# Optimization experiments

Hardware: AMD Instinct MI355X
Metric: run time of the kernel (lower is better)

The kernel has to match this reference:

```python
import jax, jax.numpy as jnp
import numpy as np

EPS = 1e-5
N_POINTS = 262144
K_VOL = 27
N_PAIRS = 65536
C_IN = 64
C_OUT = 64


def setup_inputs() -> dict:
    key = jax.random.key(0)
    k1, k2, k3, k4 = jax.random.split(key, 4)
    std = 1.0 / np.sqrt(C_IN * K_VOL)  # matches reset_parameters uniform(-std, std)
    input_feat = jax.random.normal(k1, (N_POINTS, C_IN), dtype=jnp.float32)
    input_coord = jax.random.randint(k2, (N_POINTS, 4), 0, 1024, dtype=jnp.int32)
    input_cmap = jnp.arange(N_POINTS, dtype=jnp.int32)
    input_kmap = jax.random.randint(k3, (K_VOL, N_PAIRS, 2), 0, N_POINTS, dtype=jnp.int32)
    weight = jax.random.uniform(k4, (K_VOL, C_IN, C_OUT), dtype=jnp.float32,
                                minval=-std, maxval=std)
    bn_weight = jnp.ones((C_OUT,), dtype=jnp.float32)
    bn_bias = jnp.zeros((C_OUT,), dtype=jnp.float32)
    return {
        "input_feat": input_feat,
        "input_coord": input_coord,
        "input_cmap": input_cmap,
        "input_kmap": input_kmap,
        "weight": weight,
        "bn_weight": bn_weight,
        "bn_bias": bn_bias,
    }


def reference(input_feat, input_coord, input_cmap, input_kmap, weight, bn_weight, bn_bias):
    # Sparse 3D conv (stride=1 -> output coords == input coords) via
    # gather -> per-offset GEMM -> scatter-add, then training-mode BN + ReLU.
    n_out = input_feat.shape[0]
    in_idx = input_kmap[..., 0]   # [K, P]
    out_idx = input_kmap[..., 1]  # [K, P]
    gathered = input_feat[in_idx]                         # [K, P, Cin]
    partial = jnp.einsum('kpc,kcd->kpd', gathered, weight)  # [K, P, Cout]
    out = jax.ops.segment_sum(partial.reshape(-1, partial.shape[-1]),
                              out_idx.reshape(-1), num_segments=n_out)  # [N, Cout]
    # BatchNorm1d, training mode (batch statistics, biased variance)
    mean = jnp.mean(out, axis=0)
    var = jnp.var(out, axis=0)
    y = (out - mean) * jax.lax.rsqrt(var + EPS) * bn_weight + bn_bias
    return jax.nn.relu(y)
```

## Files before the change

kernel.cpp:

```cpp
#include <hip/hip_runtime.h>

#define NPTS 262144
#define KVOL 27
#define NPAIRS 65536
#define TP (KVOL*NPAIRS)
#define CH 64
#define NT32 (NPTS/32)
#define NSEG (NT32*32)
#define NBLK2 2048
#define MAXR 12

typedef __attribute__((ext_vector_type(8))) short bf16x8;
typedef __attribute__((ext_vector_type(4))) float f32x4;

__device__ inline unsigned short f2bf(float x){
  unsigned int u = __float_as_uint(x);
  u += 0x7FFFu + ((u >> 16) & 1u);
  return (unsigned short)(u >> 16);
}

__device__ inline bf16x8 pack8(float4 a, float4 b){
  bf16x8 r;
  r[0]=(short)f2bf(a.x); r[1]=(short)f2bf(a.y); r[2]=(short)f2bf(a.z); r[3]=(short)f2bf(a.w);
  r[4]=(short)f2bf(b.x); r[5]=(short)f2bf(b.y); r[6]=(short)f2bf(b.z); r[7]=(short)f2bf(b.w);
  return r;
}

template<bool BF16G>
__global__ void k_pre(const float* __restrict__ feat, const float* __restrict__ w,
                      const int2* __restrict__ km, unsigned short* __restrict__ featb,
                      unsigned short* __restrict__ wpack, int* __restrict__ cnt,
                      unsigned short* __restrict__ rankb){
  int i = blockIdx.x*256 + threadIdx.x;
  if (BF16G){
    float4 v = ((const float4*)feat)[i];
    ushort4 r;
    r.x = f2bf(v.x); r.y = f2bf(v.y); r.z = f2bf(v.z); r.w = f2bf(v.w);
    ((ushort4*)featb)[i] = r;
  }
  if (i < TP){
    int2 io = km[i];
    int k = i >> 16;
    int seg = ((io.y >> 5) << 5) | k;
    int rank = atomicAdd(&cnt[seg], 1);
    rankb[i] = (unsigned short)rank;
  }
  if (i < KVOL*CH*CH){
    int j = i & 7, col = (i >> 3) & 63, kb = (i >> 9) & 7, k = i >> 12;
    wpack[i] = f2bf(w[(k*CH + kb*8 + j)*CH + col]);
  }
}

__global__ void k_assign(const int* __restrict__ cnt, int* __restrict__ gtot,
                         int2* __restrict__ segd){
  int i = blockIdx.x*256 + threadIdx.x;
  int l = threadIdx.x & 63;
  int c = cnt[i];
  int v = c;
  #pragma unroll
  for (int d = 1; d < 64; d <<= 1){ int u = __shfl_up(v, d, 64); if (l >= d) v += u; }
  int wtot = __shfl(v, 63, 64);
  int base = 0;
  if (l == 63) base = atomicAdd(gtot, wtot);
  base = __shfl(base, 63, 64);
  segd[i] = make_int2(base + v - c, c);
}

__global__ void k_scatter(const int2* __restrict__ km, const unsigned short* __restrict__ rankb,
                          const int2* __restrict__ segd, int* __restrict__ records){
  int i = blockIdx.x*256 + threadIdx.x;
  int2 io = km[i];
  int k = i >> 16;
  int seg = ((io.y >> 5) << 5) | k;
  int pos = segd[seg].x + rankb[i];
  records[pos] = io.x | ((io.y & 31) << 18);
}

template<bool BF16G>
__global__ __launch_bounds__(256, 4) void k_conv8(
    const unsigned short* __restrict__ featb, const float* __restrict__ featf,
    const unsigned short* __restrict__ wpack, const int* __restrict__ records,
    const int2* __restrict__ segd, float* __restrict__ out, float* __restrict__ partials)
{
  __shared__ int lcnt[4][32];
  __shared__ int lslot[4][MAXR*32];
  __shared__ float sred[4][2][64];

  int tid = threadIdx.x;
  int wv = tid>>6, l = tid&63, lg = l>>4, li = l&15;
  int t32 = blockIdx.x*4 + wv;
  int segbase = t32 << 5;

  const bf16x8* fb = (const bf16x8*)featb;
  const float4* ff = (const float4*)featf;
  const bf16x8* wbase = ((const bf16x8*)wpack) + lg*64 + li;

  f32x4 acc[2][4];
  #pragma unroll
  for (int rt = 0; rt < 2; rt++)
    #pragma unroll
    for (int ct = 0; ct < 4; ct++) acc[rt][ct] = (f32x4)(0.0f);

  int2 sd  = segd[segbase];
  int2 sd1 = segd[segbase + 1];
  int rec_pf = 0;
  if (l < sd.y) rec_pf = records[sd.x + l];

  for (int k = 0; k < KVOL; k++){
    int2 sd2 = segd[segbase + min(k + 2, 31)];
    int rec_nx = 0;
    if (l < sd1.y) rec_nx = records[sd1.x + l];

    int beg = sd.x, tot = sd.y;
    if (tot > 0){
      bf16x8 B[4][2];
      #pragma unroll
      for (int ct = 0; ct < 4; ct++)
        #pragma unroll
        for (int h = 0; h < 2; h++)
          B[ct][h] = wbase[k*512 + h*256 + ct*16];

      int rec = rec_pf;
      for (int c0 = 0; c0 < tot; c0 += 64){
        int cc = min(64, tot - c0);
        if (c0 > 0 && l < cc) rec = records[beg + c0 + l];
        if (l < 32) lcnt[wv][l] = 0;
        if (l < cc){
          int slot = (rec >> 18) & 31;
          int rank = atomicAdd(&lcnt[wv][slot], 1);
          if (rank < MAXR) lslot[wv][rank*32 + slot] = rec;
        }
        int cnt0 = min(lcnt[wv][li], MAXR);
        int cnt1 = min(lcnt[wv][16 + li], MAXR);
        int nr = max(cnt0, cnt1);
        #pragma unroll
        for (int d = 1; d < 16; d <<= 1) nr = max(nr, __shfl_xor(nr, d, 64));

        for (int rb = 0; rb < nr; rb += 2){
          int recA0 = lslot[wv][rb*32 + li];
          int recA1 = lslot[wv][rb*32 + 16 + li];
          int recB0 = lslot[wv][min(rb+1, MAXR-1)*32 + li];
          int recB1 = lslot[wv][min(rb+1, MAXR-1)*32 + 16 + li];
          bool vA0 = (rb < cnt0), vA1 = (rb < cnt1);
          bool vB0 = (rb+1 < cnt0), vB1 = (rb+1 < cnt1);
          bf16x8 a00 = (bf16x8)(short)0, a01 = (bf16x8)(short)0;
          bf16x8 a10 = (bf16x8)(short)0, a11 = (bf16x8)(short)0;
          bf16x8 b00 = (bf16x8)(short)0, b01 = (bf16x8)(short)0;
          bf16x8 b10 = (bf16x8)(short)0, b11 = (bf16x8)(short)0;
          if (vA0){
            int in = recA0 & 0x3FFFF;
            if (BF16G){ a00 = fb[in*8 + lg]; a01 = fb[in*8 + 4 + lg]; }
            else {
              float4 u0 = ff[in*16 + lg*2],     u1 = ff[in*16 + lg*2 + 1];
              float4 u2 = ff[in*16 + 8 + lg*2], u3 = ff[in*16 + 8 + lg*2 + 1];
              a00 = pack8(u0, u1); a01 = pack8(u2, u3);
            }
          }
          if (vA1){
            int in = recA1 & 0x3FFFF;
            if (BF16G){ a10 = fb[in*8 + lg]; a11 = fb[in*8 + 4 + lg]; }
            else {
              float4 u0 = ff[in*16 + lg*2],     u1 = ff[in*16 + lg*2 + 1];
              float4 u2 = ff[in*16 + 8 + lg*2], u3 = ff[in*16 + 8 + lg*2 + 1];
              a10 = pack8(u0, u1); a11 = pack8(u2, u3);
            }
          }
          if (vB0){
            int in = recB0 & 0x3FFFF;
            if (BF16G){ b00 = fb[in*8 + lg]; b01 = fb[in*8 + 4 + lg]; }
            else {
              float4 u0 = ff[in*16 + lg*2],     u1 = ff[in*16 + lg*2 + 1];
              float4 u2 = ff[in*16 + 8 + lg*2], u3 = ff[in*16 + 8 + lg*2 + 1];
              b00 = pack8(u0, u1); b01 = pack8(u2, u3);
            }
          }
          if (vB1){
            int in = recB1 & 0x3FFFF;
            if (BF16G){ b10 = fb[in*8 + lg]; b11 = fb[in*8 + 4 + lg]; }
            else {
              float4 u0 = ff[in*16 + lg*2],     u1 = ff[in*16 + lg*2 + 1];
              float4 u2 = ff[in*16 + 8 + lg*2], u3 = ff[in*16 + 8 + lg*2 + 1];
              b10 = pack8(u0, u1); b11 = pack8(u2, u3);
            }
          }
          if (__ballot(vA0)){
            #pragma unroll
            for (int ct = 0; ct < 4; ct++){
              acc[0][ct] = __builtin_amdgcn_mfma_f32_16x16x32_bf16(a00, B[ct][0], acc[0][ct], 0, 0, 0);
              acc[0][ct] = __builtin_amdgcn_mfma_f32_16x16x32_bf16(a01, B[ct][1], acc[0][ct], 0, 0, 0);
            }
          }
          if (__ballot(vA1)){
            #pragma unroll
            for (int ct = 0; ct < 4; ct++){
              acc[1][ct] = __builtin_amdgcn_mfma_f32_16x16x32_bf16(a10, B[ct][0], acc[1][ct], 0, 0, 0);
              acc[1][ct] = __builtin_amdgcn_mfma_f32_16x16x32_bf16(a11, B[ct][1], acc[1][ct], 0, 0, 0);
            }
          }
          if (rb + 1 < nr){
            if (__ballot(vB0)){
              #pragma unroll
              for (int ct = 0; ct < 4; ct++){
                acc[0][ct] = __builtin_amdgcn_mfma_f32_16x16x32_bf16(b00, B[ct][0], acc[0][ct], 0, 0, 0);
                acc[0][ct] = __builtin_amdgcn_mfma_f32_16x16x32_bf16(b01, B[ct][1], acc[0][ct], 0, 0, 0);
              }
            }
            if (__ballot(vB1)){
              #pragma unroll
              for (int ct = 0; ct < 4; ct++){
                acc[1][ct] = __builtin_amdgcn_mfma_f32_16x16x32_bf16(b10, B[ct][0], acc[1][ct], 0, 0, 0);
                acc[1][ct] = __builtin_amdgcn_mfma_f32_16x16x32_bf16(b11, B[ct][1], acc[1][ct], 0, 0, 0);
              }
            }
          }
        }
      }
    }
    rec_pf = rec_nx; sd = sd1; sd1 = sd2;
  }

  #pragma unroll
  for (int rt = 0; rt < 2; rt++)
    #pragma unroll
    for (int r = 0; r < 4; r++){
      int row = t32*32 + rt*16 + lg*4 + r;
      #pragma unroll
      for (int ct = 0; ct < 4; ct++)
        out[row*CH + ct*16 + li] = acc[rt][ct][r];
    }

  float s1[4], s2[4];
  #pragma unroll
  for (int ct = 0; ct < 4; ct++){
    float a1 = 0.f, a2 = 0.f;
    #pragma unroll
    for (int rt = 0; rt < 2; rt++)
      #pragma unroll
      for (int r = 0; r < 4; r++){
        float v = acc[rt][ct][r];
        a1 += v; a2 += v*v;
      }
    a1 += __shfl_xor(a1, 16, 64); a1 += __shfl_xor(a1, 32, 64);
    a2 += __shfl_xor(a2, 16, 64); a2 += __shfl_xor(a2, 32, 64);
    s1[ct] = a1; s2[ct] = a2;
  }
  __syncthreads();
  if (l < 16){
    #pragma unroll
    for (int ct = 0; ct < 4; ct++){
      sred[wv][0][ct*16 + li] = s1[ct];
      sred[wv][1][ct*16 + li] = s2[ct];
    }
  }
  __syncthreads();
  if (tid < 128){
    int h = tid >> 6, c = tid & 63;
    float p = sred[0][h][c] + sred[1][h][c] + sred[2][h][c] + sred[3][h][c];
    partials[blockIdx.x*128 + tid] = p;
  }
}

__global__ void k_statred(const float* __restrict__ partials, float* __restrict__ stats){
  __shared__ float sm_[256];
  int c = blockIdx.x;
  int t = threadIdx.x;
  float s = 0.f;
  for (int b = t; b < NBLK2; b += 256) s += partials[b*128 + c];
  sm_[t] = s;
  __syncthreads();
  for (int d = 128; d > 0; d >>= 1){
    if (t < d) sm_[t] += sm_[t+d];
    __syncthreads();
  }
  if (t == 0) stats[c] = sm_[0];
}

__global__ void k_bn(float* __restrict__ out, const float* __restrict__ stats,
                     const float* __restrict__ g, const float* __restrict__ b){
  int i = blockIdx.x * blockDim.x + threadIdx.x;
  float4 v = ((const float4*)out)[i];
  int c0 = (i * 4) & 63;
  float vals[4] = {v.x, v.y, v.z, v.w};
  float res[4];
  #pragma unroll
  for (int q = 0; q < 4; q++){
    int c = c0 + q;
    float mean = stats[c] * (1.0f/NPTS);
    float var  = stats[64+c] * (1.0f/NPTS) - mean*mean;
    float inv  = rsqrtf(var + 1e-5f);
    float y = (vals[q] - mean) * inv * g[c] + b[c];
    res[q] = fmaxf(y, 0.0f);
  }
  float4 r; r.x=res[0]; r.y=res[1]; r.z=res[2]; r.w=res[3];
  ((float4*)out)[i] = r;
}

extern "C" void kernel_launch(void* const* d_in, const int* in_sizes, int n_in,
                              void* d_out, int out_size, void* d_ws, size_t ws_size,
                              hipStream_t stream) {
  const float* feat   = (const float*)d_in[0];
  const int*   kmap   = (const int*)d_in[3];
  const float* weight = (const float*)d_in[4];
  const float* bnw    = (const float*)d_in[5];
  const float* bnb    = (const float*)d_in[6];
  float* out = (float*)d_out;

  char* ws = (char*)d_ws;
  size_t cur = 0;
  auto take = [&](size_t bytes){
    cur = (cur + 255) & ~(size_t)255;
    size_t p = cur; cur += bytes; return p;
  };
  float* stats          = (float*)(ws + take(2*CH*sizeof(float)));
  float* partials       = (float*)(ws + take((size_t)NBLK2*128*sizeof(float)));
  int* cnt              = (int*)(ws + take((size_t)(NSEG+64)*4));
  int2* segd            = (int2*)(ws + take((size_t)NSEG*8));
  unsigned short* wpack = (unsigned short*)(ws + take((size_t)KVOL*CH*CH*2));
  unsigned short* rankb = (unsigned short*)(ws + take((size_t)TP*2));
  int* records          = (int*)(ws + take((size_t)TP*4));
  size_t featb_off      = take((size_t)NPTS*CH*2);
  bool useBf16 = (ws_size >= cur);
  unsigned short* featb = (unsigned short*)(ws + featb_off);
  int* gtot = cnt + NSEG;

  hipMemsetAsync(cnt, 0, (size_t)(NSEG+64)*4, stream);

  const int2* km = (const int2*)kmap;
  if (useBf16)
    k_pre<true><<<NPTS*CH/4/256, 256, 0, stream>>>(feat, weight, km, featb, wpack, cnt, rankb);
  else
    k_pre<false><<<TP/256, 256, 0, stream>>>(feat, weight, km, featb, wpack, cnt, rankb);

  k_assign<<<NSEG/256, 256, 0, stream>>>(cnt, gtot, segd);
  k_scatter<<<TP/256, 256, 0, stream>>>(km, rankb, segd, records);

  if (useBf16)
    k_conv8<true><<<NBLK2, 256, 0, stream>>>(featb, feat, wpack, records, segd, out, partials);
  else
    k_conv8<false><<<NBLK2, 256, 0, stream>>>(featb, feat, wpack, records, segd, out, partials);

  k_statred<<<128, 256, 0, stream>>>(partials, stats);
  k_bn<<<NPTS*CH/4/256, 256, 0, stream>>>(out, stats, bnw, bnb);
}
```

Baseline: 315.1 us.

## Switch conv tile MFMA from 16x16x32 to 32x32x16 over full 32-row tile

```diff
diff --git a/kernel.cpp b/kernel.cpp
--- a/kernel.cpp
+++ b/kernel.cpp
@@ -11,7 +11,7 @@
 #define MAXR 12
 
 typedef __attribute__((ext_vector_type(8))) short bf16x8;
-typedef __attribute__((ext_vector_type(4))) float f32x4;
+typedef __attribute__((ext_vector_type(16))) float f32x16;
 
 __device__ inline unsigned short f2bf(float x){
   unsigned int u = __float_as_uint(x);
@@ -46,8 +46,9 @@
     rankb[i] = (unsigned short)rank;
   }
   if (i < KVOL*CH*CH){
-    int j = i & 7, col = (i >> 3) & 63, kb = (i >> 9) & 7, k = i >> 12;
-    wpack[i] = f2bf(w[(k*CH + kb*8 + j)*CH + col]);
+    int j = i & 7, col = (i >> 3) & 63, kh = (i >> 9) & 1, ks = (i >> 10) & 3, k = i >> 12;
+    int cin = ks*16 + kh*8 + j;
+    wpack[i] = f2bf(w[(k*CH + cin)*CH + col]);
   }
 }
 
@@ -77,7 +78,7 @@
 }
 
 template<bool BF16G>
-__global__ __launch_bounds__(256, 4) void k_conv8(
+__global__ __launch_bounds__(256, 4) void k_conv9(
     const unsigned short* __restrict__ featb, const float* __restrict__ featf,
     const unsigned short* __restrict__ wpack, const int* __restrict__ records,
     const int2* __restrict__ segd, float* __restrict__ out, float* __restrict__ partials)
@@ -87,19 +88,15 @@
   __shared__ float sred[4][2][64];
 
   int tid = threadIdx.x;
-  int wv = tid>>6, l = tid&63, lg = l>>4, li = l&15;
+  int wv = tid>>6, l = tid&63, ls = l&31, kh = l>>5;
   int t32 = blockIdx.x*4 + wv;
   int segbase = t32 << 5;
 
-  const bf16x8* fb = (const bf16x8*)featb;
+  const bf16x8* fa = ((const bf16x8*)featb) + kh;
   const float4* ff = (const float4*)featf;
-  const bf16x8* wbase = ((const bf16x8*)wpack) + lg*64 + li;
-
-  f32x4 acc[2][4];
-  #pragma unroll
-  for (int rt = 0; rt < 2; rt++)
-    #pragma unroll
-    for (int ct = 0; ct < 4; ct++) acc[rt][ct] = (f32x4)(0.0f);
+  const bf16x8* wb = ((const bf16x8*)wpack) + kh*64 + ls;
+
+  f32x16 acc0 = (f32x16)(0.0f), acc1 = (f32x16)(0.0f);
 
   int2 sd  = segd[segbase];
   int2 sd1 = segd[segbase + 1];
@@ -113,12 +110,12 @@
 
     int beg = sd.x, tot = sd.y;
     if (tot > 0){
-      bf16x8 B[4][2];
+      bf16x8 B[2][4];
       #pragma unroll
-      for (int ct = 0; ct < 4; ct++)
+      for (int ct = 0; ct < 2; ct++)
         #pragma unroll
-        for (int h = 0; h < 2; h++)
-          B[ct][h] = wbase[k*512 + h*256 + ct*16];
+        for (int ks = 0; ks < 4; ks++)
+          B[ct][ks] = wb[(k*4 + ks)*128 + ct*32];
 
       int rec = rec_pf;
       for (int c0 = 0; c0 < tot; c0 += 64){
@@ -130,89 +127,35 @@
           int rank = atomicAdd(&lcnt[wv][slot], 1);
           if (rank < MAXR) lslot[wv][rank*32 + slot] = rec;
         }
-        int cnt0 = min(lcnt[wv][li], MAXR);
-        int cnt1 = min(lcnt[wv][16 + li], MAXR);
-        int nr = max(cnt0, cnt1);
-        #pragma unroll
-        for (int d = 1; d < 16; d <<= 1) nr = max(nr, __shfl_xor(nr, d, 64));
-
-        for (int rb = 0; rb < nr; rb += 2){
-          int recA0 = lslot[wv][rb*32 + li];
-          int recA1 = lslot[wv][rb*32 + 16 + li];
-          int recB0 = lslot[wv][min(rb+1, MAXR-1)*32 + li];
-          int recB1 = lslot[wv][min(rb+1, MAXR-1)*32 + 16 + li];
-          bool vA0 = (rb < cnt0), vA1 = (rb < cnt1);
-          bool vB0 = (rb+1 < cnt0), vB1 = (rb+1 < cnt1);
-          bf16x8 a00 = (bf16x8)(short)0, a01 = (bf16x8)(short)0;
-          bf16x8 a10 = (bf16x8)(short)0, a11 = (bf16x8)(short)0;
-          bf16x8 b00 = (bf16x8)(short)0, b01 = (bf16x8)(short)0;
-          bf16x8 b10 = (bf16x8)(short)0, b11 = (bf16x8)(short)0;
-          if (vA0){
-            int in = recA0 & 0x3FFFF;
-            if (BF16G){ a00 = fb[in*8 + lg]; a01 = fb[in*8 + 4 + lg]; }
-            else {
-              float4 u0 = ff[in*16 + lg*2],     u1 = ff[in*16 + lg*2 + 1];
-              float4 u2 = ff[in*16 + 8 + lg*2], u3 = ff[in*16 + 8 + lg*2 + 1];
-              a00 = pack8(u0, u1); a01 = pack8(u2, u3);
+        int cnt_s = min(lcnt[wv][ls], MAXR);
+        for (int r = 0; r < MAXR; r++){
+          bool valid = (r < cnt_s);
+          if (__ballot(valid) == 0ull) break;
+          int rs = lslot[wv][r*32 + ls];
+          bf16x8 A0 = (bf16x8)(short)0, A1 = (bf16x8)(short)0;
+          bf16x8 A2 = (bf16x8)(short)0, A3 = (bf16x8)(short)0;
+          if (valid){
+            int in = rs & 0x3FFFF;
+            if (BF16G){
+              A0 = fa[in*8];     A1 = fa[in*8 + 2];
+              A2 = fa[in*8 + 4]; A3 = fa[in*8 + 6];
+            } else {
+              float4 u0 = ff[in*16 + kh*2],      u1 = ff[in*16 + kh*2 + 1];
+              float4 u2 = ff[in*16 + 4 + kh*2],  u3 = ff[in*16 + 4 + kh*2 + 1];
+              float4 u4 = ff[in*16 + 8 + kh*2],  u5 = ff[in*16 + 8 + kh*2 + 1];
+              float4 u6 = ff[in*16 + 12 + kh*2], u7 = ff[in*16 + 12 + kh*2 + 1];
+              A0 = pack8(u0, u1); A1 = pack8(u2, u3);
+              A2 = pack8(u4, u5); A3 = pack8(u6, u7);
             }
           }
-          if (vA1){
-            int in = recA1 & 0x3FFFF;
-            if (BF16G){ a10 = fb[in*8 + lg]; a11 = fb[in*8 + 4 + lg]; }
-            else {
-              float4 u0 = ff[in*16 + lg*2],     u1 = ff[in*16 + lg*2 + 1];
-              float4 u2 = ff[in*16 + 8 + lg*2], u3 = ff[in*16 + 8 + lg*2 + 1];
-              a10 = pack8(u0, u1); a11 = pack8(u2, u3);
-            }
-          }
-          if (vB0){
-            int in = recB0 & 0x3FFFF;
-            if (BF16G){ b00 = fb[in*8 + lg]; b01 = fb[in*8 + 4 + lg]; }
-            else {
-              float4 u0 = ff[in*16 + lg*2],     u1 = ff[in*16 + lg*2 + 1];
-              float4 u2 = ff[in*16 + 8 + lg*2], u3 = ff[in*16 + 8 + lg*2 + 1];
-              b00 = pack8(u0, u1); b01 = pack8(u2, u3);
-            }
-          }
-          if (vB1){
-            int in = recB1 & 0x3FFFF;
-            if (BF16G){ b10 = fb[in*8 + lg]; b11 = fb[in*8 + 4 + lg]; }
-            else {
-              float4 u0 = ff[in*16 + lg*2],     u1 = ff[in*16 + lg*2 + 1];
-              float4 u2 = ff[in*16 + 8 + lg*2], u3 = ff[in*16 + 8 + lg*2 + 1];
-              b10 = pack8(u0, u1); b11 = pack8(u2, u3);
-            }
-          }
-          if (__ballot(vA0)){
-            #pragma unroll
-            for (int ct = 0; ct < 4; ct++){
-              acc[0][ct] = __builtin_amdgcn_mfma_f32_16x16x32_bf16(a00, B[ct][0], acc[0][ct], 0, 0, 0);
-              acc[0][ct] = __builtin_amdgcn_mfma_f32_16x16x32_bf16(a01, B[ct][1], acc[0][ct], 0, 0, 0);
-            }
-          }
-          if (__ballot(vA1)){
-            #pragma unroll
-            for (int ct = 0; ct < 4; ct++){
-              acc[1][ct] = __builtin_amdgcn_mfma_f32_16x16x32_bf16(a10, B[ct][0], acc[1][ct], 0, 0, 0);
-              acc[1][ct] = __builtin_amdgcn_mfma_f32_16x16x32_bf16(a11, B[ct][1], acc[1][ct], 0, 0, 0);
-            }
-          }
-          if (rb + 1 < nr){
-            if (__ballot(vB0)){
-              #pragma unroll
-              for (int ct = 0; ct < 4; ct++){
-                acc[0][ct] = __builtin_amdgcn_mfma_f32_16x16x32_bf16(b00, B[ct][0], acc[0][ct], 0, 0, 0);
-                acc[0][ct] = __builtin_amdgcn_mfma_f32_16x16x32_bf16(b01, B[ct][1], acc[0][ct], 0, 0, 0);
-              }
-            }
-            if (__ballot(vB1)){
-              #pragma unroll
-              for (int ct = 0; ct < 4; ct++){
-                acc[1][ct] = __builtin_amdgcn_mfma_f32_16x16x32_bf16(b10, B[ct][0], acc[1][ct], 0, 0, 0);
-                acc[1][ct] = __builtin_amdgcn_mfma_f32_16x16x32_bf16(b11, B[ct][1], acc[1][ct], 0, 0, 0);
-              }
-            }
-          }
+          acc0 = __builtin_amdgcn_mfma_f32_32x32x16_bf16(A0, B[0][0], acc0, 0, 0, 0);
+          acc1 = __builtin_amdgcn_mfma_f32_32x32x16_bf16(A0, B[1][0], acc1, 0, 0, 0);
+          acc0 = __builtin_amdgcn_mfma_f32_32x32x16_bf16(A1, B[0][1], acc0, 0, 0, 0);
+          acc1 = __builtin_amdgcn_mfma_f32_32x32x16_bf16(A1, B[1][1], acc1, 0, 0, 0);
+          acc0 = __builtin_amdgcn_mfma_f32_32x32x16_bf16(A2, B[0][2], acc0, 0, 0, 0);
+          acc1 = __builtin_amdgcn_mfma_f32_32x32x16_bf16(A2, B[1][2], acc1, 0, 0, 0);
+          acc0 = __builtin_amdgcn_mfma_f32_32x32x16_bf16(A3, B[0][3], acc0, 0, 0, 0);
+          acc1 = __builtin_amdgcn_mfma_f32_32x32x16_bf16(A3, B[1][3], acc1, 0, 0, 0);
         }
       }
     }
@@ -220,37 +163,27 @@
   }
 
   #pragma unroll
-  for (int rt = 0; rt < 2; rt++)
-    #pragma unroll
-    for (int r = 0; r < 4; r++){
-      int row = t32*32 + rt*16 + lg*4 + r;
-      #pragma unroll
-      for (int ct = 0; ct < 4; ct++)
-        out[row*CH + ct*16 + li] = acc[rt][ct][r];
-    }
-
-  float s1[4], s2[4];
-  #pragma unroll
-  for (int ct = 0; ct < 4; ct++){
-    float a1 = 0.f, a2 = 0.f;
-    #pragma unroll
-    for (int rt = 0; rt < 2; rt++)
-      #pragma unroll
-      for (int r = 0; r < 4; r++){
-        float v = acc[rt][ct][r];
-        a1 += v; a2 += v*v;
-      }
-    a1 += __shfl_xor(a1, 16, 64); a1 += __shfl_xor(a1, 32, 64);
-    a2 += __shfl_xor(a2, 16, 64); a2 += __shfl_xor(a2, 32, 64);
-    s1[ct] = a1; s2[ct] = a2;
-  }
+  for (int p = 0; p < 16; p++){
+    int row = t32*32 + (p & 3) + 8*(p >> 2) + 4*kh;
+    out[row*CH + ls]      = acc0[p];
+    out[row*CH + 32 + ls] = acc1[p];
+  }
+
+  float s10 = 0.f, s20 = 0.f, s11 = 0.f, s21 = 0.f;
+  #pragma unroll
+  for (int p = 0; p < 16; p++){
+    float v0 = acc0[p], v1 = acc1[p];
+    s10 += v0; s20 += v0*v0;
+    s11 += v1; s21 += v1*v1;
+  }
+  s10 += __shfl_xor(s10, 32, 64); s20 += __shfl_xor(s20, 32, 64);
+  s11 += __shfl_xor(s11, 32, 64); s21 += __shfl_xor(s21, 32, 64);
   __syncthreads();
-  if (l < 16){
-    #pragma unroll
-    for (int ct = 0; ct < 4; ct++){
-      sred[wv][0][ct*16 + li] = s1[ct];
-      sred[wv][1][ct*16 + li] = s2[ct];
-    }
+  if (l < 32){
+    sred[wv][0][ls]      = s10;
+    sred[wv][0][32 + ls] = s11;
+    sred[wv][1][ls]      = s20;
+    sred[wv][1][32 + ls] = s21;
   }
   __syncthreads();
   if (tid < 128){
@@ -335,9 +268,9 @@
   k_scatter<<<TP/256, 256, 0, stream>>>(km, rankb, segd, records);
 
   if (useBf16)
-    k_conv8<true><<<NBLK2, 256, 0, stream>>>(featb, feat, wpack, records, segd, out, partials);
+    k_conv9<true><<<NBLK2, 256, 0, stream>>>(featb, feat, wpack, records, segd, out, partials);
   else
-    k_conv8<false><<<NBLK2, 256, 0, stream>>>(featb, feat, wpack, records, segd, out, partials);
+    k_conv9<false><<<NBLK2, 256, 0, stream>>>(featb, feat, wpack, records, segd, out, partials);
 
   k_statred<<<128, 256, 0, stream>>>(partials, stats);
   k_bn<<<NPTS*CH/4/256, 256, 0, stream>>>(out, stats, bnw, bnb);
```

Result: slower. 346.3 us (+9.9%).

## Double-buffer per-offset slot tables and prefetch next offset's first-rank gathers

Applied to the files above, without the earlier changes.

```diff
diff --git a/kernel.cpp b/kernel.cpp
--- a/kernel.cpp
+++ b/kernel.cpp
@@ -77,13 +77,13 @@
 }
 
 template<bool BF16G>
-__global__ __launch_bounds__(256, 4) void k_conv8(
+__global__ __launch_bounds__(256, 4) void k_conv10(
     const unsigned short* __restrict__ featb, const float* __restrict__ featf,
     const unsigned short* __restrict__ wpack, const int* __restrict__ records,
     const int2* __restrict__ segd, float* __restrict__ out, float* __restrict__ partials)
 {
-  __shared__ int lcnt[4][32];
-  __shared__ int lslot[4][MAXR*32];
+  __shared__ int lcnt[4][2][32];
+  __shared__ int lslot[4][2][MAXR*32];
   __shared__ float sred[4][2][64];
 
   int tid = threadIdx.x;
@@ -101,17 +101,64 @@
     #pragma unroll
     for (int ct = 0; ct < 4; ct++) acc[rt][ct] = (f32x4)(0.0f);
 
-  int2 sd  = segd[segbase];
-  int2 sd1 = segd[segbase + 1];
-  int rec_pf = 0;
-  if (l < sd.y) rec_pf = records[sd.x + l];
+  auto buildTable = [&](int buf, int rec, int cc){
+    if (l < 32) lcnt[wv][buf][l] = 0;
+    if (l < cc){
+      int slot = (rec >> 18) & 31;
+      int rank = atomicAdd(&lcnt[wv][buf][slot], 1);
+      if (rank < MAXR) lslot[wv][buf][rank*32 + slot] = rec;
+    }
+  };
+  auto gatherA = [&](int rec, bool v, bf16x8& X0, bf16x8& X1){
+    X0 = (bf16x8)(short)0; X1 = (bf16x8)(short)0;
+    if (v){
+      int in = rec & 0x3FFFF;
+      if (BF16G){ X0 = fb[in*8 + lg]; X1 = fb[in*8 + 4 + lg]; }
+      else {
+        float4 u0 = ff[in*16 + lg*2],     u1 = ff[in*16 + lg*2 + 1];
+        float4 u2 = ff[in*16 + 8 + lg*2], u3 = ff[in*16 + 8 + lg*2 + 1];
+        X0 = pack8(u0, u1); X1 = pack8(u2, u3);
+      }
+    }
+  };
+  auto mfma8 = [&](bf16x8 X0, bf16x8 X1, f32x4 (&arow)[4], bf16x8 (&B)[4][2]){
+    #pragma unroll
+    for (int ct = 0; ct < 4; ct++){
+      arow[ct] = __builtin_amdgcn_mfma_f32_16x16x32_bf16(X0, B[ct][0], arow[ct], 0, 0, 0);
+      arow[ct] = __builtin_amdgcn_mfma_f32_16x16x32_bf16(X1, B[ct][1], arow[ct], 0, 0, 0);
+    }
+  };
+
+  int2 sdA = segd[segbase + 0];
+  int2 sdB = segd[segbase + 1];
+  int2 sdC = segd[segbase + 2];
+  int rec_cur = 0;
+  if (l < sdA.y) rec_cur = records[sdA.x + l];
+  buildTable(0, rec_cur, min(64, sdA.y));
+  int pc0 = min(lcnt[wv][0][li], MAXR), pc1 = min(lcnt[wv][0][16 + li], MAXR);
+  bf16x8 P00, P01, P10, P11;
+  gatherA(lslot[wv][0][li],      pc0 > 0, P00, P01);
+  gatherA(lslot[wv][0][16 + li], pc1 > 0, P10, P11);
+  int rec_nx = 0;
+  if (l < sdB.y) rec_nx = records[sdB.x + l];
 
   for (int k = 0; k < KVOL; k++){
-    int2 sd2 = segd[segbase + min(k + 2, 31)];
-    int rec_nx = 0;
-    if (l < sd1.y) rec_nx = records[sd1.x + l];
-
-    int beg = sd.x, tot = sd.y;
+    int cb = k & 1, nb = cb ^ 1;
+
+    int ncnt0 = 0, ncnt1 = 0;
+    bf16x8 N00, N01, N10, N11;
+    N00 = N01 = N10 = N11 = (bf16x8)(short)0;
+    if (k + 1 < KVOL && sdB.y > 0){
+      buildTable(nb, rec_nx, min(64, sdB.y));
+      ncnt0 = min(lcnt[wv][nb][li], MAXR);
+      ncnt1 = min(lcnt[wv][nb][16 + li], MAXR);
+      gatherA(lslot[wv][nb][li],      ncnt0 > 0, N00, N01);
+      gatherA(lslot[wv][nb][16 + li], ncnt1 > 0, N10, N11);
+    }
+    int rec2 = 0;
+    if (l < sdC.y) rec2 = records[sdC.x + l];
+
+    int tot = sdA.y;
     if (tot > 0){
       bf16x8 B[4][2];
       #pragma unroll
@@ -120,103 +167,43 @@
         for (int h = 0; h < 2; h++)
           B[ct][h] = wbase[k*512 + h*256 + ct*16];
 
-      int rec = rec_pf;
-      for (int c0 = 0; c0 < tot; c0 += 64){
+      if (__ballot(pc0 > 0)) mfma8(P00, P01, acc[0], B);
+      if (__ballot(pc1 > 0)) mfma8(P10, P11, acc[1], B);
+      for (int r = 1; r < MAXR; r++){
+        bool v0 = (r < pc0), v1 = (r < pc1);
+        if (__ballot(v0 || v1) == 0ull) break;
+        int rr0 = lslot[wv][cb][r*32 + li];
+        int rr1 = lslot[wv][cb][r*32 + 16 + li];
+        bf16x8 X00, X01, X10, X11;
+        gatherA(rr0, v0, X00, X01);
+        gatherA(rr1, v1, X10, X11);
+        if (__ballot(v0)) mfma8(X00, X01, acc[0], B);
+        if (__ballot(v1)) mfma8(X10, X11, acc[1], B);
+      }
+      for (int c0 = 64; c0 < tot; c0 += 64){
         int cc = min(64, tot - c0);
-        if (c0 > 0 && l < cc) rec = records[beg + c0 + l];
-        if (l < 32) lcnt[wv][l] = 0;
-        if (l < cc){
-          int slot = (rec >> 18) & 31;
-          int rank = atomicAdd(&lcnt[wv][slot], 1);
-          if (rank < MAXR) lslot[wv][rank*32 + slot] = rec;
-        }
-        int cnt0 = min(lcnt[wv][li], MAXR);
-        int cnt1 = min(lcnt[wv][16 + li], MAXR);
-        int nr = max(cnt0, cnt1);
-        #pragma unroll
-        for (int d = 1; d < 16; d <<= 1) nr = max(nr, __shfl_xor(nr, d, 64));
-
-        for (int rb = 0; rb < nr; rb += 2){
-          int recA0 = lslot[wv][rb*32 + li];
-          int recA1 = lslot[wv][rb*32 + 16 + li];
-          int recB0 = lslot[wv][min(rb+1, MAXR-1)*32 + li];
-          int recB1 = lslot[wv][min(rb+1, MAXR-1)*32 + 16 + li];
-          bool vA0 = (rb < cnt0), vA1 = (rb < cnt1);
-          bool vB0 = (rb+1 < cnt0), vB1 = (rb+1 < cnt1);
-          bf16x8 a00 = (bf16x8)(short)0, a01 = (bf16x8)(short)0;
-          bf16x8 a10 = (bf16x8)(short)0, a11 = (bf16x8)(short)0;
-          bf16x8 b00 = (bf16x8)(short)0, b01 = (bf16x8)(short)0;
-          bf16x8 b10 = (bf16x8)(short)0, b11 = (bf16x8)(short)0;
-          if (vA0){
-            int in = recA0 & 0x3FFFF;
-            if (BF16G){ a00 = fb[in*8 + lg]; a01 = fb[in*8 + 4 + lg]; }
-            else {
-              float4 u0 = ff[in*16 + lg*2],     u1 = ff[in*16 + lg*2 + 1];
-              float4 u2 = ff[in*16 + 8 + lg*2], u3 = ff[in*16 + 8 + lg*2 + 1];
-              a00 = pack8(u0, u1); a01 = pack8(u2, u3);
-            }
-          }
-          if (vA1){
-            int in = recA1 & 0x3FFFF;
-            if (BF16G){ a10 = fb[in*8 + lg]; a11 = fb[in*8 + 4 + lg]; }
-            else {
-              float4 u0 = ff[in*16 + lg*2],     u1 = ff[in*16 + lg*2 + 1];
-              float4 u2 = ff[in*16 + 8 + lg*2], u3 = ff[in*16 + 8 + lg*2 + 1];
-              a10 = pack8(u0, u1); a11 = pack8(u2, u3);
-            }
-          }
-          if (vB0){
-            int in = recB0 & 0x3FFFF;
-            if (BF16G){ b00 = fb[in*8 + lg]; b01 = fb[in*8 + 4 + lg]; }
-            else {
-              float4 u0 = ff[in*16 + lg*2],     u1 = ff[in*16 + lg*2 + 1];
-              float4 u2 = ff[in*16 + 8 + lg*2], u3 = ff[in*16 + 8 + lg*2 + 1];
-              b00 = pack8(u0, u1); b01 = pack8(u2, u3);
-            }
-          }
-          if (vB1){
-            int in = recB1 & 0x3FFFF;
-            if (BF16G){ b10 = fb[in*8 + lg]; b11 = fb[in*8 + 4 + lg]; }
-            else {
-              float4 u0 = ff[in*16 + lg*2],     u1 = ff[in*16 + lg*2 + 1];
-              float4 u2 = ff[in*16 + 8 + lg*2], u3 = ff[in*16 + 8 + lg*2 + 1];
-              b10 = pack8(u0, u1); b11 = pack8(u2, u3);
-            }
-          }
-          if (__ballot(vA0)){
-            #pragma unroll
-            for (int ct = 0; ct < 4; ct++){
-              acc[0][ct] = __builtin_amdgcn_mfma_f32_16x16x32_bf16(a00, B[ct][0], acc[0][ct], 0, 0, 0);
-              acc[0][ct] = __builtin_amdgcn_mfma_f32_16x16x32_bf16(a01, B[ct][1], acc[0][ct], 0, 0, 0);
-            }
-          }
-          if (__ballot(vA1)){
-            #pragma unroll
-            for (int ct = 0; ct < 4; ct++){
-              acc[1][ct] = __builtin_amdgcn_mfma_f32_16x16x32_bf16(a10, B[ct][0], acc[1][ct], 0, 0, 0);
-              acc[1][ct] = __builtin_amdgcn_mfma_f32_16x16x32_bf16(a11, B[ct][1], acc[1][ct], 0, 0, 0);
-            }
-          }
-          if (rb + 1 < nr){
-            if (__ballot(vB0)){
-              #pragma unroll
-              for (int ct = 0; ct < 4; ct++){
-                acc[0][ct] = __builtin_amdgcn_mfma_f32_16x16x32_bf16(b00, B[ct][0], acc[0][ct], 0, 0, 0);
-                acc[0][ct] = __builtin_amdgcn_mfma_f32_16x16x32_bf16(b01, B[ct][1], acc[0][ct], 0, 0, 0);
-              }
-            }
-            if (__ballot(vB1)){
-              #pragma unroll
-              for (int ct = 0; ct < 4; ct++){
-                acc[1][ct] = __builtin_amdgcn_mfma_f32_16x16x32_bf16(b10, B[ct][0], acc[1][ct], 0, 0, 0);
-                acc[1][ct] = __builtin_amdgcn_mfma_f32_16x16x32_bf16(b11, B[ct][1], acc[1][ct], 0, 0, 0);
-              }
-            }
-          }
+        int rec = 0;
+        if (l < cc) rec = records[sdA.x + c0 + l];
+        buildTable(cb, rec, cc);
+        int q0 = min(lcnt[wv][cb][li], MAXR), q1 = min(lcnt[wv][cb][16 + li], MAXR);
+        for (int r = 0; r < MAXR; r++){
+          bool v0 = (r < q0), v1 = (r < q1);
+          if (__ballot(v0 || v1) == 0ull) break;
+          int rr0 = lslot[wv][cb][r*32 + li];
+          int rr1 = lslot[wv][cb][r*32 + 16 + li];
+          bf16x8 X00, X01, X10, X11;
+          gatherA(rr0, v0, X00, X01);
+          gatherA(rr1, v1, X10, X11);
+          if (__ballot(v0)) mfma8(X00, X01, acc[0], B);
+          if (__ballot(v1)) mfma8(X10, X11, acc[1], B);
         }
       }
     }
-    rec_pf = rec_nx; sd = sd1; sd1 = sd2;
+
+    sdA = sdB; sdB = sdC; sdC = segd[segbase + min(k + 3, 31)];
+    rec_nx = rec2;
+    pc0 = ncnt0; pc1 = ncnt1;
+    P00 = N00; P01 = N01; P10 = N10; P11 = N11;
   }
 
   #pragma unroll
@@ -335,9 +322,9 @@
   k_scatter<<<TP/256, 256, 0, stream>>>(km, rankb, segd, records);
 
   if (useBf16)
-    k_conv8<true><<<NBLK2, 256, 0, stream>>>(featb, feat, wpack, records, segd, out, partials);
+    k_conv10<true><<<NBLK2, 256, 0, stream>>>(featb, feat, wpack, records, segd, out, partials);
   else
-    k_conv8<false><<<NBLK2, 256, 0, stream>>>(featb, feat, wpack, records, segd, out, partials);
+    k_conv10<false><<<NBLK2, 256, 0, stream>>>(featb, feat, wpack, records, segd, out, partials);
 
   k_statred<<<128, 256, 0, stream>>>(partials, stats);
   k_bn<<<NPTS*CH/4/256, 256, 0, stream>>>(out, stats, bnw, bnb);
```

Measured after the change: 1.168 ms. 3.71x slower.

## Replace counting-sort bucketing with fixed-capacity segment buckets plus spill list

Applied to the files above, without the earlier changes.

```diff
diff --git a/kernel.cpp b/kernel.cpp
--- a/kernel.cpp
+++ b/kernel.cpp
@@ -9,6 +9,7 @@
 #define NSEG (NT32*32)
 #define NBLK2 2048
 #define MAXR 12
+#define SPILLMAX 131072
 
 typedef __attribute__((ext_vector_type(8))) short bf16x8;
 typedef __attribute__((ext_vector_type(4))) float f32x4;
@@ -27,10 +28,11 @@
 }
 
 template<bool BF16G>
-__global__ void k_pre(const float* __restrict__ feat, const float* __restrict__ w,
-                      const int2* __restrict__ km, unsigned short* __restrict__ featb,
-                      unsigned short* __restrict__ wpack, int* __restrict__ cnt,
-                      unsigned short* __restrict__ rankb){
+__global__ void k_pre2(const float* __restrict__ feat, const float* __restrict__ w,
+                       const int2* __restrict__ km, unsigned short* __restrict__ featb,
+                       unsigned short* __restrict__ wpack, int* __restrict__ cnt,
+                       int* __restrict__ records, int2* __restrict__ spill,
+                       int* __restrict__ spillcnt, int C){
   int i = blockIdx.x*256 + threadIdx.x;
   if (BF16G){
     float4 v = ((const float4*)feat)[i];
@@ -43,7 +45,12 @@
     int k = i >> 16;
     int seg = ((io.y >> 5) << 5) | k;
     int rank = atomicAdd(&cnt[seg], 1);
-    rankb[i] = (unsigned short)rank;
+    int rec = io.x | ((io.y & 31) << 18);
+    if (rank < C) records[seg*C + rank] = rec;
+    else {
+      int sp = atomicAdd(spillcnt, 1);
+      if (sp < SPILLMAX) spill[sp] = make_int2(seg, rec);
+    }
   }
   if (i < KVOL*CH*CH){
     int j = i & 7, col = (i >> 3) & 63, kb = (i >> 9) & 7, k = i >> 12;
@@ -51,36 +58,13 @@
   }
 }
 
-__global__ void k_assign(const int* __restrict__ cnt, int* __restrict__ gtot,
-                         int2* __restrict__ segd){
-  int i = blockIdx.x*256 + threadIdx.x;
-  int l = threadIdx.x & 63;
-  int c = cnt[i];
-  int v = c;
-  #pragma unroll
-  for (int d = 1; d < 64; d <<= 1){ int u = __shfl_up(v, d, 64); if (l >= d) v += u; }
-  int wtot = __shfl(v, 63, 64);
-  int base = 0;
-  if (l == 63) base = atomicAdd(gtot, wtot);
-  base = __shfl(base, 63, 64);
-  segd[i] = make_int2(base + v - c, c);
-}
-
-__global__ void k_scatter(const int2* __restrict__ km, const unsigned short* __restrict__ rankb,
-                          const int2* __restrict__ segd, int* __restrict__ records){
-  int i = blockIdx.x*256 + threadIdx.x;
-  int2 io = km[i];
-  int k = i >> 16;
-  int seg = ((io.y >> 5) << 5) | k;
-  int pos = segd[seg].x + rankb[i];
-  records[pos] = io.x | ((io.y & 31) << 18);
-}
-
 template<bool BF16G>
-__global__ __launch_bounds__(256, 4) void k_conv8(
+__global__ __launch_bounds__(256, 4) void k_conv12(
     const unsigned short* __restrict__ featb, const float* __restrict__ featf,
     const unsigned short* __restrict__ wpack, const int* __restrict__ records,
-    const int2* __restrict__ segd, float* __restrict__ out, float* __restrict__ partials)
+    const int* __restrict__ cnt, const int2* __restrict__ spill,
+    const int* __restrict__ spillcnt, int C,
+    float* __restrict__ out, float* __restrict__ partials)
 {
   __shared__ int lcnt[4][32];
   __shared__ int lslot[4][MAXR*32];
@@ -101,17 +85,18 @@
     #pragma unroll
     for (int ct = 0; ct < 4; ct++) acc[rt][ct] = (f32x4)(0.0f);
 
-  int2 sd  = segd[segbase];
-  int2 sd1 = segd[segbase + 1];
+  int myc = (l < KVOL) ? cnt[segbase + l] : 0;
+
+  int tot_cur = __builtin_amdgcn_readlane(myc, 0);
   int rec_pf = 0;
-  if (l < sd.y) rec_pf = records[sd.x + l];
+  if (l < min(tot_cur, C)) rec_pf = records[segbase*C + l];
 
   for (int k = 0; k < KVOL; k++){
-    int2 sd2 = segd[segbase + min(k + 2, 31)];
+    int tot = tot_cur;
+    int tot_nx = (k < KVOL-1) ? __builtin_amdgcn_readlane(myc, k+1) : 0;
     int rec_nx = 0;
-    if (l < sd1.y) rec_nx = records[sd1.x + l];
-
-    int beg = sd.x, tot = sd.y;
+    if (l < min(tot_nx, C)) rec_nx = records[(segbase + k + 1)*C + l];
+
     if (tot > 0){
       bf16x8 B[4][2];
       #pragma unroll
@@ -120,103 +105,103 @@
         for (int h = 0; h < 2; h++)
           B[ct][h] = wbase[k*512 + h*256 + ct*16];
 
-      int rec = rec_pf;
-      for (int c0 = 0; c0 < tot; c0 += 64){
-        int cc = min(64, tot - c0);
-        if (c0 > 0 && l < cc) rec = records[beg + c0 + l];
-        if (l < 32) lcnt[wv][l] = 0;
-        if (l < cc){
-          int slot = (rec >> 18) & 31;
-          int rank = atomicAdd(&lcnt[wv][slot], 1);
-          if (rank < MAXR) lslot[wv][rank*32 + slot] = rec;
-        }
-        int cnt0 = min(lcnt[wv][li], MAXR);
-        int cnt1 = min(lcnt[wv][16 + li], MAXR);
-        int nr = max(cnt0, cnt1);
+      if (l < 32) lcnt[wv][l] = 0;
+      int bcnt = min(tot, C);
+      if (l < bcnt){
+        int slot = (rec_pf >> 18) & 31;
+        int rank = atomicAdd(&lcnt[wv][slot], 1);
+        if (rank < MAXR) lslot[wv][rank*32 + slot] = rec_pf;
+      }
+      int cnt0 = min(lcnt[wv][li], MAXR);
+      int cnt1 = min(lcnt[wv][16 + li], MAXR);
+
+      for (int r = 0; r < MAXR; r++){
+        bool v0 = (r < cnt0), v1 = (r < cnt1);
+        if (__ballot(v0 || v1) == 0ull) break;
+        int rr0 = lslot[wv][r*32 + li];
+        int rr1 = lslot[wv][r*32 + 16 + li];
+        bf16x8 X00 = (bf16x8)(short)0, X01 = (bf16x8)(short)0;
+        bf16x8 X10 = (bf16x8)(short)0, X11 = (bf16x8)(short)0;
+        if (v0){
+          int in = rr0 & 0x3FFFF;
+          if (BF16G){ X00 = fb[in*8 + lg]; X01 = fb[in*8 + 4 + lg]; }
+          else {
+            float4 u0 = ff[in*16 + lg*2],     u1 = ff[in*16 + lg*2 + 1];
+            float4 u2 = ff[in*16 + 8 + lg*2], u3 = ff[in*16 + 8 + lg*2 + 1];
+            X00 = pack8(u0, u1); X01 = pack8(u2, u3);
+          }
+        }
+        if (v1){
+          int in = rr1 & 0x3FFFF;
+          if (BF16G){ X10 = fb[in*8 + lg]; X11 = fb[in*8 + 4 + lg]; }
+          else {
+            float4 u0 = ff[in*16 + lg*2],     u1 = ff[in*16 + lg*2 + 1];
+            float4 u2 = ff[in*16 + 8 + lg*2], u3 = ff[in*16 + 8 + lg*2 + 1];
+            X10 = pack8(u0, u1); X11 = pack8(u2, u3);
+          }
+        }
+        if (__ballot(v0)){
+          #pragma unroll
+          for (int ct = 0; ct < 4; ct++){
+            acc[0][ct] = __builtin_amdgcn_mfma_f32_16x16x32_bf16(X00, B[ct][0], acc[0][ct], 0, 0, 0);
+            acc[0][ct] = __builtin_amdgcn_mfma_f32_16x16x32_bf16(X01, B[ct][1], acc[0][ct], 0, 0, 0);
+          }
+        }
+        if (__ballot(v1)){
+          #pragma unroll
+          for (int ct = 0; ct < 4; ct++){
+            acc[1][ct] = __builtin_amdgcn_mfma_f32_16x16x32_bf16(X10, B[ct][0], acc[1][ct], 0, 0, 0);
+            acc[1][ct] = __builtin_amdgcn_mfma_f32_16x16x32_bf16(X11, B[ct][1], acc[1][ct], 0, 0, 0);
+          }
+        }
+      }
+    }
+    rec_pf = rec_nx; tot_cur = tot_nx;
+  }
+
+  int nsp = min(spillcnt[0], SPILLMAX);
+  for (int s0 = 0; s0 < nsp; s0 += 64){
+    int idx = s0 + l;
+    int2 e = make_int2(-1, 0);
+    if (idx < nsp) e = spill[idx];
+    unsigned long long m = __ballot((e.x >= 0) && ((e.x >> 5) == t32));
+    while (m){
+      int j = __ffsll((long long)m) - 1; m &= m - 1;
+      int sj = __shfl(e.x, j, 64);
+      int rj = __shfl(e.y, j, 64);
+      int kk = sj & 31;
+      int slot = (rj >> 18) & 31, hh = slot >> 4, sl = slot & 15;
+      bf16x8 Bs[4][2];
+      #pragma unroll
+      for (int ct = 0; ct < 4; ct++)
         #pragma unroll
-        for (int d = 1; d < 16; d <<= 1) nr = max(nr, __shfl_xor(nr, d, 64));
-
-        for (int rb = 0; rb < nr; rb += 2){
-          int recA0 = lslot[wv][rb*32 + li];
-          int recA1 = lslot[wv][rb*32 + 16 + li];
-          int recB0 = lslot[wv][min(rb+1, MAXR-1)*32 + li];
-          int recB1 = lslot[wv][min(rb+1, MAXR-1)*32 + 16 + li];
-          bool vA0 = (rb < cnt0), vA1 = (rb < cnt1);
-          bool vB0 = (rb+1 < cnt0), vB1 = (rb+1 < cnt1);
-          bf16x8 a00 = (bf16x8)(short)0, a01 = (bf16x8)(short)0;
-          bf16x8 a10 = (bf16x8)(short)0, a11 = (bf16x8)(short)0;
-          bf16x8 b00 = (bf16x8)(short)0, b01 = (bf16x8)(short)0;
-          bf16x8 b10 = (bf16x8)(short)0, b11 = (bf16x8)(short)0;
-          if (vA0){
-            int in = recA0 & 0x3FFFF;
-            if (BF16G){ a00 = fb[in*8 + lg]; a01 = fb[in*8 + 4 + lg]; }
-            else {
-              float4 u0 = ff[in*16 + lg*2],     u1 = ff[in*16 + lg*2 + 1];
-              float4 u2 = ff[in*16 + 8 + lg*2], u3 = ff[in*16 + 8 + lg*2 + 1];
-              a00 = pack8(u0, u1); a01 = pack8(u2, u3);
-            }
-          }
-          if (vA1){
-            int in = recA1 & 0x3FFFF;
-            if (BF16G){ a10 = fb[in*8 + lg]; a11 = fb[in*8 + 4 + lg]; }
-            else {
-              float4 u0 = ff[in*16 + lg*2],     u1 = ff[in*16 + lg*2 + 1];
-              float4 u2 = ff[in*16 + 8 + lg*2], u3 = ff[in*16 + 8 + lg*2 + 1];
-              a10 = pack8(u0, u1); a11 = pack8(u2, u3);
-            }
-          }
-          if (vB0){
-            int in = recB0 & 0x3FFFF;
-            if (BF16G){ b00 = fb[in*8 + lg]; b01 = fb[in*8 + 4 + lg]; }
-            else {
-              float4 u0 = ff[in*16 + lg*2],     u1 = ff[in*16 + lg*2 + 1];
-              float4 u2 = ff[in*16 + 8 + lg*2], u3 = ff[in*16 + 8 + lg*2 + 1];
-              b00 = pack8(u0, u1); b01 = pack8(u2, u3);
-            }
-          }
-          if (vB1){
-            int in = recB1 & 0x3FFFF;
-            if (BF16G){ b10 = fb[in*8 + lg]; b11 = fb[in*8 + 4 + lg]; }
-            else {
-              float4 u0 = ff[in*16 + lg*2],     u1 = ff[in*16 + lg*2 + 1];
-              float4 u2 = ff[in*16 + 8 + lg*2], u3 = ff[in*16 + 8 + lg*2 + 1];
-              b10 = pack8(u0, u1); b11 = pack8(u2, u3);
-            }
-          }
-          if (__ballot(vA0)){
-            #pragma unroll
-            for (int ct = 0; ct < 4; ct++){
-              acc[0][ct] = __builtin_amdgcn_mfma_f32_16x16x32_bf16(a00, B[ct][0], acc[0][ct], 0, 0, 0);
-              acc[0][ct] = __builtin_amdgcn_mfma_f32_16x16x32_bf16(a01, B[ct][1], acc[0][ct], 0, 0, 0);
-            }
-          }
-          if (__ballot(vA1)){
-            #pragma unroll
-            for (int ct = 0; ct < 4; ct++){
-              acc[1][ct] = __builtin_amdgcn_mfma_f32_16x16x32_bf16(a10, B[ct][0], acc[1][ct], 0, 0, 0);
-              acc[1][ct] = __builtin_amdgcn_mfma_f32_16x16x32_bf16(a11, B[ct][1], acc[1][ct], 0, 0, 0);
-            }
-          }
-          if (rb + 1 < nr){
-            if (__ballot(vB0)){
-              #pragma unroll
-              for (int ct = 0; ct < 4; ct++){
-                acc[0][ct] = __builtin_amdgcn_mfma_f32_16x16x32_bf16(b00, B[ct][0], acc[0][ct], 0, 0, 0);
-                acc[0][ct] = __builtin_amdgcn_mfma_f32_16x16x32_bf16(b01, B[ct][1], acc[0][ct], 0, 0, 0);
-              }
-            }
-            if (__ballot(vB1)){
-              #pragma unroll
-              for (int ct = 0; ct < 4; ct++){
-                acc[1][ct] = __builtin_amdgcn_mfma_f32_16x16x32_bf16(b10, B[ct][0], acc[1][ct], 0, 0, 0);
-                acc[1][ct] = __builtin_amdgcn_mfma_f32_16x16x32_bf16(b11, B[ct][1], acc[1][ct], 0, 0, 0);
-              }
-            }
-          }
-        }
-      }
-    }
-    rec_pf = rec_nx; sd = sd1; sd1 = sd2;
+        for (int h = 0; h < 2; h++)
+          Bs[ct][h] = wbase[kk*512 + h*256 + ct*16];
+      bool v = (li == sl);
+      bf16x8 X0 = (bf16x8)(short)0, X1 = (bf16x8)(short)0;
+      if (v){
+        int in = rj & 0x3FFFF;
+        if (BF16G){ X0 = fb[in*8 + lg]; X1 = fb[in*8 + 4 + lg]; }
+        else {
+          float4 u0 = ff[in*16 + lg*2],     u1 = ff[in*16 + lg*2 + 1];
+          float4 u2 = ff[in*16 + 8 + lg*2], u3 = ff[in*16 + 8 + lg*2 + 1];
+          X0 = pack8(u0, u1); X1 = pack8(u2, u3);
+        }
+      }
+      if (hh == 0){
+        #pragma unroll
+        for (int ct = 0; ct < 4; ct++){
+          acc[0][ct] = __builtin_amdgcn_mfma_f32_16x16x32_bf16(X0, Bs[ct][0], acc[0][ct], 0, 0, 0);
+          acc[0][ct] = __builtin_amdgcn_mfma_f32_16x16x32_bf16(X1, Bs[ct][1], acc[0][ct], 0, 0, 0);
+        }
+      } else {
+        #pragma unroll
+        for (int ct = 0; ct < 4; ct++){
+          acc[1][ct] = __builtin_amdgcn_mfma_f32_16x16x32_bf16(X0, Bs[ct][0], acc[1][ct], 0, 0, 0);
+          acc[1][ct] = __builtin_amdgcn_mfma_f32_16x16x32_bf16(X1, Bs[ct][1], acc[1][ct], 0, 0, 0);
+        }
+      }
+    }
   }
 
   #pragma unroll
@@ -314,30 +299,38 @@
   float* stats          = (float*)(ws + take(2*CH*sizeof(float)));
   float* partials       = (float*)(ws + take((size_t)NBLK2*128*sizeof(float)));
   int* cnt              = (int*)(ws + take((size_t)(NSEG+64)*4));
-  int2* segd            = (int2*)(ws + take((size_t)NSEG*8));
+  int2* spill           = (int2*)(ws + take((size_t)SPILLMAX*8));
   unsigned short* wpack = (unsigned short*)(ws + take((size_t)KVOL*CH*CH*2));
-  unsigned short* rankb = (unsigned short*)(ws + take((size_t)TP*2));
-  int* records          = (int*)(ws + take((size_t)TP*4));
-  size_t featb_off      = take((size_t)NPTS*CH*2);
-  bool useBf16 = (ws_size >= cur);
-  unsigned short* featb = (unsigned short*)(ws + featb_off);
-  int* gtot = cnt + NSEG;
+  size_t base = cur;
+  size_t featb_bytes = (size_t)NPTS*CH*2;
+  int C = 16;
+  bool useBf16 = false;
+  {
+    size_t avail = (ws_size > base + featb_bytes + 512) ? (ws_size - base - featb_bytes - 512) : 0;
+    size_t cmax = avail / ((size_t)NSEG*4);
+    if (cmax >= 11){ useBf16 = true; C = (int)((cmax < 16) ? cmax : 16); }
+  }
+  int* records          = (int*)(ws + take((size_t)NSEG*(useBf16 ? C : 16)*4));
+  if (!useBf16) C = 16;
+  unsigned short* featb = (unsigned short*)(ws + take(featb_bytes));
+  int* spillcnt = cnt + NSEG;
 
   hipMemsetAsync(cnt, 0, (size_t)(NSEG+64)*4, stream);
 
   const int2* km = (const int2*)kmap;
   if (useBf16)
-    k_pre<true><<<NPTS*CH/4/256, 256, 0, stream>>>(feat, weight, km, featb, wpack, cnt, rankb);
+    k_pre2<true><<<NPTS*CH/4/256, 256, 0, stream>>>(feat, weight, km, featb, wpack, cnt,
+                                                    records, spill, spillcnt, C);
   else
-    k_pre<false><<<TP/256, 256, 0, stream>>>(feat, weight, km, featb, wpack, cnt, rankb);
-
-  k_assign<<<NSEG/256, 256, 0, stream>>>(cnt, gtot, segd);
-  k_scatter<<<TP/256, 256, 0, stream>>>(km, rankb, segd, records);
+    k_pre2<false><<<TP/256, 256, 0, stream>>>(feat, weight, km, featb, wpack, cnt,
+                                              records, spill, spillcnt, C);
 
   if (useBf16)
-    k_conv8<true><<<NBLK2, 256, 0, stream>>>(featb, feat, wpack, records, segd, out, partials);
+    k_conv12<true><<<NBLK2, 256, 0, stream>>>(featb, feat, wpack, records, cnt, spill,
+                                              spillcnt, C, out, partials);
   else
-    k_conv8<false><<<NBLK2, 256, 0, stream>>>(featb, feat, wpack, records, segd, out, partials);
+    k_conv12<false><<<NBLK2, 256, 0, stream>>>(featb, feat, wpack, records, cnt, spill,
+                                               spillcnt, C, out, partials);
 
   k_statred<<<128, 256, 0, stream>>>(partials, stats);
   k_bn<<<NPTS*CH/4/256, 256, 0, stream>>>(out, stats, bnw, bnb);
```

Measured after the change: 269.1 us. -14.6%, faster.
